# Performance work log

Measured on AMD Instinct MI355X. Metric: run time of the kernel, lower is better.

Reference implementation:

```python
import jax, jax.numpy as jnp
import numpy as np

MID = 256

def setup_inputs() -> dict:
    key = jax.random.key(0)
    ks = jax.random.split(key, 6)
    s = 1.0 / np.sqrt(MID)
    u = lambda k, shape: jax.random.uniform(k, shape, jnp.float32, -s, s)
    return {
        "W_ih": u(ks[0], (4 * MID, 2)),
        "W_hh": u(ks[1], (4 * MID, MID)),
        "b_ih": u(ks[2], (4 * MID,)),
        "b_hh": u(ks[3], (4 * MID,)),
        "W_out": u(ks[4], (1, MID)),
        "b_out": u(ks[5], (1,)),
        "sequence_dim": 48,
        "sequence_num": 512,
    }

def reference(W_ih, W_hh, b_ih, b_hh, W_out, b_out, sequence_dim, sequence_num):
    # obs is 2-D -> torch nn.LSTM treats it as UNBATCHED: (L=sequence_num, H_in=2),
    # hidden state (mid,) per layer, carried across outer iterations.
    N = sequence_num
    mid = W_hh.shape[1]
    b = b_ih + b_hh  # fuse the two LSTM biases

    def lstm(hc, obs):
        # obs: (N, 2) time-major unbatched sequence
        def step(carry, x):
            h, c = carry
            g = W_ih @ x + W_hh @ h + b          # (4*mid,)
            i, f, gg, o = jnp.split(g, 4)         # torch gate order i,f,g,o
            c = jax.nn.sigmoid(f) * c + jax.nn.sigmoid(i) * jnp.tanh(gg)
            h = jax.nn.sigmoid(o) * jnp.tanh(c)
            return (h, c), h
        hc, hs = jax.lax.scan(step, hc, obs)
        return hc, hs                              # hs: (N, mid)

    def outer(carry, k):
        hc, samp, prob = carry
        obs = jnp.concatenate([samp, prob], axis=1)  # (N, 2)
        hc, hs = lstm(hc, obs)
        p = jax.nn.sigmoid(hs @ W_out.T + b_out)     # (N, 1)
        smp = jax.random.bernoulli(k, p).astype(p.dtype)
        lp = smp * jnp.log(p) + (1.0 - smp) * jnp.log1p(-p)        # Bernoulli log_prob
        ent = -(p * jnp.log(p) + (1.0 - p) * jnp.log1p(-p))        # Bernoulli entropy
        return (hc, smp, p), (smp[:, 0], lp[:, 0], ent[:, 0])

    key = jax.random.key(42)
    keys = jax.random.split(key, sequence_dim - 1)
    h0 = (jnp.zeros((mid,), W_hh.dtype), jnp.zeros((mid,), W_hh.dtype))
    z = jnp.zeros((N, 1), W_hh.dtype)
    _, (ss, lps, ents) = jax.lax.scan(outer, (h0, z, z), keys)

    samples = jnp.concatenate([jnp.zeros((1, N), ss.dtype), ss], axis=0)  # (T, N)
    samples = samples.T.astype(jnp.int32)                                  # (N, T)
    logprobs = lps.sum(0)
    logprobs = logprobs - logprobs.mean()
    entropies = ents.mean(0)
    return samples, logprobs, entropies
```

## Files before the change

### kernel.cpp

```cpp
#include <hip/hip_runtime.h>
#include <stdint.h>


#define MID      256
#define NOUT     48
#define NSEQ     512
#define NOUTER   47
#define NSTEP    (NOUTER * NSEQ)
#define NBLK     16
#define MAGIC_V  0x1234ABCDu
#define LOG2E    1.4426950408889634f

__device__ __forceinline__ uint32_t rotl32(uint32_t x, int d) {
  return (x << d) | (x >> (32 - d));
}

__device__ __forceinline__ void threefry2x32(uint32_t k0, uint32_t k1,
                                             uint32_t x0, uint32_t x1,
                                             uint32_t& o0, uint32_t& o1) {
  uint32_t ks2 = k0 ^ k1 ^ 0x1BD11BDAu;
  uint32_t v0 = x0 + k0, v1 = x1 + k1;
#define TF_R(r) { v0 += v1; v1 = rotl32(v1, r); v1 ^= v0; }
  TF_R(13) TF_R(15) TF_R(26) TF_R(6)
  v0 += k1;  v1 += ks2 + 1u;
  TF_R(17) TF_R(29) TF_R(16) TF_R(24)
  v0 += ks2; v1 += k0 + 2u;
  TF_R(13) TF_R(15) TF_R(26) TF_R(6)
  v0 += k0;  v1 += k1 + 3u;
  TF_R(17) TF_R(29) TF_R(16) TF_R(24)
  v0 += k1;  v1 += ks2 + 4u;
  TF_R(13) TF_R(15) TF_R(26) TF_R(6)
  v0 += ks2; v1 += k0 + 5u;
#undef TF_R
  o0 = v0; o1 = v1;
}

__device__ __forceinline__ float sigf(float x) { return 1.0f / (1.0f + expf(-x)); }

__device__ __forceinline__ uint64_t packht(float h, uint32_t tag) {
  return ((uint64_t)tag << 32) | (uint64_t)__float_as_uint(h);
}

__global__ __launch_bounds__(256, 1)
void arlstm_kernel(const float* __restrict__ W_ih, const float* __restrict__ W_hh,
                   const float* __restrict__ b_ih, const float* __restrict__ b_hh,
                   const float* __restrict__ W_out, const float* __restrict__ b_out,
                   float* __restrict__ out, uint64_t* __restrict__ ws) {
  uint64_t* h_hist = ws;
  float*    obsbuf = (float*)(ws + 512 * 256);
  uint32_t* p_prog = (uint32_t*)(obsbuf + 2 * 512 * 2);
  uint32_t* magic  = p_prog + 16;

  const int tid = threadIdx.x;
  const int blk = blockIdx.x;

  __shared__ __align__(16) float hstage[256];
  __shared__ float plds[4][64];
  __shared__ float obs_lds[2];
  __shared__ float lp_acc[512];
  __shared__ float ent_acc[512];
  __shared__ float red[256];

  if (blk == NBLK) {
    __hip_atomic_store(&h_hist[tid], 0ull, __ATOMIC_RELAXED, __HIP_MEMORY_SCOPE_AGENT);
    if (tid < 16)
      __hip_atomic_store(&p_prog[tid], 0u, __ATOMIC_RELAXED, __HIP_MEMORY_SCOPE_AGENT);
    out[(tid)       * NOUT] = 0.0f;
    out[(tid + 256) * NOUT] = 0.0f;
    lp_acc[tid] = 0.0f;  lp_acc[tid + 256] = 0.0f;
    ent_acc[tid] = 0.0f; ent_acc[tid + 256] = 0.0f;
    __threadfence();
    __syncthreads();
    if (tid == 0)
      __hip_atomic_store(magic, MAGIC_V, __ATOMIC_RELEASE, __HIP_MEMORY_SCOPE_AGENT);

    const int w    = tid >> 6;
    const int lane = tid & 63;
    const float wo0 = W_out[lane * 4 + 0], wo1 = W_out[lane * 4 + 1];
    const float wo2 = W_out[lane * 4 + 2], wo3 = W_out[lane * 4 + 3];
    const float bo = b_out[0];

    for (int s = w + 1; s <= NSTEP; s += 4) {
      const int k = (s - 1) >> 9;
      const int t = (s - 1) & 511;
      uint64_t* src = h_hist + (uint64_t)(s & 511) * 256 + lane * 4;
      uint64_t v0, v1, v2, v3;
      for (;;) {
        v0 = __hip_atomic_load(src + 0, __ATOMIC_RELAXED, __HIP_MEMORY_SCOPE_AGENT);
        v1 = __hip_atomic_load(src + 1, __ATOMIC_RELAXED, __HIP_MEMORY_SCOPE_AGENT);
        v2 = __hip_atomic_load(src + 2, __ATOMIC_RELAXED, __HIP_MEMORY_SCOPE_AGENT);
        v3 = __hip_atomic_load(src + 3, __ATOMIC_RELAXED, __HIP_MEMORY_SCOPE_AGENT);
        int ok = ((uint32_t)(v0 >> 32) == (uint32_t)s) &
                 ((uint32_t)(v1 >> 32) == (uint32_t)s) &
                 ((uint32_t)(v2 >> 32) == (uint32_t)s) &
                 ((uint32_t)(v3 >> 32) == (uint32_t)s);
        if (__all(ok)) break;
      }
      float zp = fmaf(__uint_as_float((uint32_t)v0), wo0,
                 fmaf(__uint_as_float((uint32_t)v1), wo1,
                 fmaf(__uint_as_float((uint32_t)v2), wo2,
                      __uint_as_float((uint32_t)v3) * wo3)));
      zp += __shfl_xor(zp, 1);
      zp += __shfl_xor(zp, 2);
      zp += __shfl_xor(zp, 4);
      zp += __shfl_xor(zp, 8);
      zp += __shfl_xor(zp, 16);
      zp += __shfl_xor(zp, 32);
      const float p = sigf(zp + bo);

      uint32_t ka, kb, c1, c2;
      threefry2x32(0u, 42u, 0u, (uint32_t)k, ka, kb);
      threefry2x32(ka, kb, 0u, (uint32_t)t, c1, c2);
      const uint32_t bits = c1 ^ c2;
      const float u = __uint_as_float((bits >> 9) | 0x3f800000u) - 1.0f;
      const float smp = (u < p) ? 1.0f : 0.0f;

      if (lane == 0) {
        uint32_t* ob = (uint32_t*)(obsbuf + ((k + 1) & 1) * (512 * 2) + t * 2);
        __hip_atomic_store(&ob[0], __float_as_uint(smp), __ATOMIC_RELAXED, __HIP_MEMORY_SCOPE_AGENT);
        __hip_atomic_store(&ob[1], __float_as_uint(p),   __ATOMIC_RELAXED, __HIP_MEMORY_SCOPE_AGENT);
        __hip_atomic_store(&p_prog[w], (uint32_t)s, __ATOMIC_RELEASE, __HIP_MEMORY_SCOPE_AGENT);
        out[t * NOUT + (k + 1)] = smp;
        const float lg = logf(p), lg1 = log1pf(-p);
        lp_acc[t]  += (smp > 0.5f) ? lg : lg1;
        ent_acc[t] -= (p * lg + (1.0f - p) * lg1);
      }
    }
    __syncthreads();
    red[tid] = lp_acc[tid] + lp_acc[tid + 256];
    __syncthreads();
    for (int off = 128; off > 0; off >>= 1) {
      if (tid < off) red[tid] += red[tid + off];
      __syncthreads();
    }
    const float mean = red[0] * (1.0f / 512.0f);
    out[24576 + tid]        = lp_acc[tid]        - mean;
    out[24576 + 256 + tid]  = lp_acc[tid + 256]  - mean;
    out[25088 + tid]        = ent_acc[tid]       * (1.0f / 47.0f);
    out[25088 + 256 + tid]  = ent_acc[tid + 256] * (1.0f / 47.0f);
  } else {
    const int part = tid >> 6;
    const int r    = tid & 63;
    const int gate = r >> 4;
    const int jloc = r & 15;
    const int row  = gate * 256 + blk * 16 + jloc;

    float wreg[64];
#pragma unroll
    for (int c = 0; c < 64; ++c)
      wreg[c] = W_hh[row * 256 + part * 64 + c];

    float bb = 0.f, wx0 = 0.f, wx1 = 0.f, mconst = 0.f, ml = 0.f, ad = 0.f;
    if (tid < 64) {
      const int g4 = tid >> 4;
      const int rr = g4 * 256 + blk * 16 + (tid & 15);
      bb  = b_ih[rr] + b_hh[rr];
      wx0 = W_ih[rr * 2 + 0];
      wx1 = W_ih[rr * 2 + 1];
      mconst = (g4 == 2) ? (-2.0f * LOG2E) : (-LOG2E);
      ml     = (g4 == 2) ? 2.0f : 1.0f;
      ad     = (g4 == 2) ? -1.0f : 0.0f;
    }

    if (tid == 0) {
      while (__hip_atomic_load(magic, __ATOMIC_ACQUIRE, __HIP_MEMORY_SCOPE_AGENT) != MAGIC_V) {}
    }
    __syncthreads();

    float c_st = 0.0f;
    const int jglob = blk * 16 + (tid & 15);

    for (int s = 1; s <= NSTEP; ++s) {
      const int k = (s - 1) >> 9;
      const int t = (s - 1) & 511;

      float samp = 0.0f, pv = 0.0f;
      if (tid == 255 && k > 0) {
        const uint32_t X = (uint32_t)((k - 1) * 512 + t + 1);
        while (__hip_atomic_load(&p_prog[t & 3], __ATOMIC_ACQUIRE, __HIP_MEMORY_SCOPE_AGENT) < X) {}
        uint32_t* ob = (uint32_t*)(obsbuf + (k & 1) * (512 * 2) + t * 2);
        samp = __uint_as_float(__hip_atomic_load(&ob[0], __ATOMIC_RELAXED, __HIP_MEMORY_SCOPE_AGENT));
        pv   = __uint_as_float(__hip_atomic_load(&ob[1], __ATOMIC_RELAXED, __HIP_MEMORY_SCOPE_AGENT));
      }

      {
        uint64_t* src = h_hist + (uint64_t)((s - 1) & 511) * 256 + tid;
        const uint32_t want = (uint32_t)(s - 1);
        uint64_t v = __hip_atomic_load(src, __ATOMIC_RELAXED, __HIP_MEMORY_SCOPE_AGENT);
        if ((uint32_t)(v >> 32) != want) {
          uint64_t a = __hip_atomic_load(src, __ATOMIC_RELAXED, __HIP_MEMORY_SCOPE_AGENT);
          uint64_t b = __hip_atomic_load(src, __ATOMIC_RELAXED, __HIP_MEMORY_SCOPE_AGENT);
          for (;;) {
            if ((uint32_t)(a >> 32) == want) { v = a; break; }
            a = __hip_atomic_load(src, __ATOMIC_RELAXED, __HIP_MEMORY_SCOPE_AGENT);
            if ((uint32_t)(b >> 32) == want) { v = b; break; }
            b = __hip_atomic_load(src, __ATOMIC_RELAXED, __HIP_MEMORY_SCOPE_AGENT);
          }
        }
        hstage[tid] = __uint_as_float((uint32_t)v);
      }
      if (tid == 255) { obs_lds[0] = samp; obs_lds[1] = pv; }
      __syncthreads();

      float a0 = 0.f, a1 = 0.f, a2 = 0.f, a3 = 0.f;
      const float4* hs4 = (const float4*)(hstage + part * 64);
#pragma unroll
      for (int i = 0; i < 16; ++i) {
        const float4 hv = hs4[i];
        a0 = fmaf(wreg[4 * i + 0], hv.x, a0);
        a1 = fmaf(wreg[4 * i + 1], hv.y, a1);
        a2 = fmaf(wreg[4 * i + 2], hv.z, a2);
        a3 = fmaf(wreg[4 * i + 3], hv.w, a3);
      }
      plds[part][r] = (a0 + a1) + (a2 + a3);
      __syncthreads();

      if (tid < 64) {
        const float sx = obs_lds[0], px = obs_lds[1];
        const float base = wx0 * sx + wx1 * px + bb;
        const float gv = ((plds[0][tid] + plds[1][tid]) +
                          (plds[2][tid] + plds[3][tid])) + base;
        const float e   = __builtin_amdgcn_exp2f(gv * mconst);
        const float y   = __builtin_amdgcn_rcpf(1.0f + e);
        const float act = __builtin_fmaf(ml, y, ad);
        const int j = tid & 15;
        const float a_f = __shfl(act, j + 16, 64);
        const float a_g = __shfl(act, j + 32, 64);
        const float a_o = __shfl(act, j + 48, 64);
        if (tid < 16) {
          const float t1 = a_f * c_st;
          const float t2 = act * a_g;
          c_st = t1 + t2;
          const float ec = __builtin_amdgcn_exp2f(c_st * (-2.0f * LOG2E));
          const float yc = __builtin_amdgcn_rcpf(1.0f + ec);
          const float th = __builtin_fmaf(2.0f, yc, -1.0f);
          const float hnew = a_o * th;
          __hip_atomic_store(&h_hist[(uint64_t)(s & 511) * 256 + jglob],
                             packht(hnew, (uint32_t)s),
                             __ATOMIC_RELAXED, __HIP_MEMORY_SCOPE_AGENT);
        }
      }
    }
  }
}

extern "C" void kernel_launch(void* const* d_in, const int* in_sizes, int n_in,
                              void* d_out, int out_size, void* d_ws, size_t ws_size,
                              hipStream_t stream) {
  const float* W_ih  = (const float*)d_in[0];
  const float* W_hh  = (const float*)d_in[1];
  const float* b_ih  = (const float*)d_in[2];
  const float* b_hh  = (const float*)d_in[3];
  const float* W_out = (const float*)d_in[4];
  const float* b_out = (const float*)d_in[5];
  float* out = (float*)d_out;
  uint64_t* ws = (uint64_t*)d_ws;

  arlstm_kernel<<<dim3(NBLK + 1), dim3(256), 0, stream>>>(
      W_ih, W_hh, b_ih, b_hh, W_out, b_out, out, ws);
}
```

Before: 31.82 ms.

## Remove second block barrier via in-wave gate reduction and prefetched observation ring

Each wave now owns four hidden units across all four gates, so the K-split partial sums are combined with wave shuffles instead of an LDS exchange and a second __syncthreads per step. Observations from the sampler block are prefetched 16 steps ahead by one wave into a double-buffered LDS ring, which takes the p_prog spin-wait off the critical path. The h stage is double-buffered, and a block writes its own new h values straight into LDS rather than re-reading them from global memory. In exchange the indexing and prefetch-phase logic are more intricate, which raises the risk of ordering bugs.

```diff
diff --git a/kernel.cpp b/kernel.cpp
--- a/kernel.cpp
+++ b/kernel.cpp
@@ -10,6 +10,8 @@
 #define NBLK     16
 #define MAGIC_V  0x1234ABCDu
 #define LOG2E    1.4426950408889634f
+
+#define LD_REL(p) __hip_atomic_load((p), __ATOMIC_RELAXED, __HIP_MEMORY_SCOPE_AGENT)
 
 __device__ __forceinline__ uint32_t rotl32(uint32_t x, int d) {
   return (x << d) | (x >> (32 - d));
@@ -50,13 +52,13 @@
   float*    obsbuf = (float*)(ws + 512 * 256);
   uint32_t* p_prog = (uint32_t*)(obsbuf + 2 * 512 * 2);
   uint32_t* magic  = p_prog + 16;
+  uint64_t* ob64   = (uint64_t*)obsbuf;
 
   const int tid = threadIdx.x;
   const int blk = blockIdx.x;
 
-  __shared__ __align__(16) float hstage[256];
-  __shared__ float plds[4][64];
-  __shared__ float obs_lds[2];
+  __shared__ __align__(16) float hstage[2][256];
+  __shared__ __align__(16) float ring[2][16][2];
   __shared__ float lp_acc[512];
   __shared__ float ent_acc[512];
   __shared__ float red[256];
@@ -86,10 +88,10 @@
       uint64_t* src = h_hist + (uint64_t)(s & 511) * 256 + lane * 4;
       uint64_t v0, v1, v2, v3;
       for (;;) {
-        v0 = __hip_atomic_load(src + 0, __ATOMIC_RELAXED, __HIP_MEMORY_SCOPE_AGENT);
-        v1 = __hip_atomic_load(src + 1, __ATOMIC_RELAXED, __HIP_MEMORY_SCOPE_AGENT);
-        v2 = __hip_atomic_load(src + 2, __ATOMIC_RELAXED, __HIP_MEMORY_SCOPE_AGENT);
-        v3 = __hip_atomic_load(src + 3, __ATOMIC_RELAXED, __HIP_MEMORY_SCOPE_AGENT);
+        v0 = LD_REL(src + 0);
+        v1 = LD_REL(src + 1);
+        v2 = LD_REL(src + 2);
+        v3 = LD_REL(src + 3);
         int ok = ((uint32_t)(v0 >> 32) == (uint32_t)s) &
                  ((uint32_t)(v1 >> 32) == (uint32_t)s) &
                  ((uint32_t)(v2 >> 32) == (uint32_t)s) &
@@ -139,27 +141,30 @@
     out[25088 + tid]        = ent_acc[tid]       * (1.0f / 47.0f);
     out[25088 + 256 + tid]  = ent_acc[tid + 256] * (1.0f / 47.0f);
   } else {
-    const int part = tid >> 6;
-    const int r    = tid & 63;
-    const int gate = r >> 4;
-    const int jloc = r & 15;
-    const int row  = gate * 256 + blk * 16 + jloc;
+    const int lane6 = tid & 63;
+    const int wv    = tid >> 6;
+    const int p     = lane6 & 3;
+    const int js    = (lane6 >> 2) & 3;
+    const int gate  = lane6 >> 4;
+    const int jl    = 4 * wv + js;
+    const int jglob = blk * 16 + jl;
+    const int rr    = gate * 256 + blk * 16 + jl;
 
     float wreg[64];
 #pragma unroll
     for (int c = 0; c < 64; ++c)
-      wreg[c] = W_hh[row * 256 + part * 64 + c];
-
-    float bb = 0.f, wx0 = 0.f, wx1 = 0.f, mconst = 0.f, ml = 0.f, ad = 0.f;
-    if (tid < 64) {
-      const int g4 = tid >> 4;
-      const int rr = g4 * 256 + blk * 16 + (tid & 15);
-      bb  = b_ih[rr] + b_hh[rr];
-      wx0 = W_ih[rr * 2 + 0];
-      wx1 = W_ih[rr * 2 + 1];
-      mconst = (g4 == 2) ? (-2.0f * LOG2E) : (-LOG2E);
-      ml     = (g4 == 2) ? 2.0f : 1.0f;
-      ad     = (g4 == 2) ? -1.0f : 0.0f;
+      wreg[c] = W_hh[rr * 256 + p * 64 + c];
+
+    const float bb  = b_ih[rr] + b_hh[rr];
+    const float wx0 = W_ih[rr * 2 + 0];
+    const float wx1 = W_ih[rr * 2 + 1];
+    const float mconst = (gate == 2) ? (-2.0f * LOG2E) : (-LOG2E);
+    const float ml     = (gate == 2) ? 2.0f : 1.0f;
+    const float ad     = (gate == 2) ? -1.0f : 0.0f;
+
+    if (tid < 16) {
+      ring[0][tid][0] = 0.f; ring[0][tid][1] = 0.f;
+      ring[1][tid][0] = 0.f; ring[1][tid][1] = 0.f;
     }
 
     if (tid == 0) {
@@ -168,42 +173,68 @@
     __syncthreads();
 
     float c_st = 0.0f;
-    const int jglob = blk * 16 + (tid & 15);
+    const bool own = (tid >= blk * 16) && (tid < blk * 16 + 16);
+
+    int      pf_tgt = 0, pf_need = 0;
+    uint32_t pf_ppv = 0;
+    uint64_t pf_ov  = 0;
 
     for (int s = 1; s <= NSTEP; ++s) {
-      const int k = (s - 1) >> 9;
-      const int t = (s - 1) & 511;
-
-      float samp = 0.0f, pv = 0.0f;
-      if (tid == 255 && k > 0) {
-        const uint32_t X = (uint32_t)((k - 1) * 512 + t + 1);
-        while (__hip_atomic_load(&p_prog[t & 3], __ATOMIC_ACQUIRE, __HIP_MEMORY_SCOPE_AGENT) < X) {}
-        uint32_t* ob = (uint32_t*)(obsbuf + (k & 1) * (512 * 2) + t * 2);
-        samp = __uint_as_float(__hip_atomic_load(&ob[0], __ATOMIC_RELAXED, __HIP_MEMORY_SCOPE_AGENT));
-        pv   = __uint_as_float(__hip_atomic_load(&ob[1], __ATOMIC_RELAXED, __HIP_MEMORY_SCOPE_AGENT));
-      }
-
-      {
+      const int ph = (s - 1) & 15;
+
+      if (wv == 3) {
+        if (ph == 0) {
+          pf_tgt  = s + 16 + lane6;
+          pf_need = 0;
+          if (lane6 < 16 && pf_tgt > NSEQ && pf_tgt <= NSTEP) {
+            pf_need = pf_tgt - NSEQ;
+            pf_ppv  = LD_REL(&p_prog[(pf_need - 1) & 3]);
+          }
+        } else if (ph == 1) {
+          bool ok = (pf_need == 0) || (pf_ppv >= (uint32_t)pf_need);
+          while (!__all(ok)) {
+            if (!ok) pf_ppv = LD_REL(&p_prog[(pf_need - 1) & 3]);
+            ok = (pf_need == 0) || (pf_ppv >= (uint32_t)pf_need);
+          }
+          pf_ov = 0;
+          if (lane6 < 16 && pf_need != 0) {
+            const int kk = (pf_tgt - 1) >> 9;
+            const int tt = (pf_tgt - 1) & 511;
+            pf_ov = LD_REL(ob64 + (kk & 1) * 512 + tt);
+          }
+        } else if (ph == 2) {
+          if (lane6 < 16) {
+            const int par = (((s - 3) >> 4) + 1) & 1;
+            ring[par][lane6][0] = __uint_as_float((uint32_t)pf_ov);
+            ring[par][lane6][1] = __uint_as_float((uint32_t)(pf_ov >> 32));
+          }
+        }
+      }
+
+      if (s == 1 || !own) {
         uint64_t* src = h_hist + (uint64_t)((s - 1) & 511) * 256 + tid;
         const uint32_t want = (uint32_t)(s - 1);
-        uint64_t v = __hip_atomic_load(src, __ATOMIC_RELAXED, __HIP_MEMORY_SCOPE_AGENT);
+        uint64_t v = LD_REL(src);
         if ((uint32_t)(v >> 32) != want) {
-          uint64_t a = __hip_atomic_load(src, __ATOMIC_RELAXED, __HIP_MEMORY_SCOPE_AGENT);
-          uint64_t b = __hip_atomic_load(src, __ATOMIC_RELAXED, __HIP_MEMORY_SCOPE_AGENT);
+          uint64_t q0 = LD_REL(src), q1 = LD_REL(src);
+          uint64_t q2 = LD_REL(src), q3 = LD_REL(src);
           for (;;) {
-            if ((uint32_t)(a >> 32) == want) { v = a; break; }
-            a = __hip_atomic_load(src, __ATOMIC_RELAXED, __HIP_MEMORY_SCOPE_AGENT);
-            if ((uint32_t)(b >> 32) == want) { v = b; break; }
-            b = __hip_atomic_load(src, __ATOMIC_RELAXED, __HIP_MEMORY_SCOPE_AGENT);
+            if ((uint32_t)(q0 >> 32) == want) { v = q0; break; }
+            q0 = LD_REL(src);
+            if ((uint32_t)(q1 >> 32) == want) { v = q1; break; }
+            q1 = LD_REL(src);
+            if ((uint32_t)(q2 >> 32) == want) { v = q2; break; }
+            q2 = LD_REL(src);
+            if ((uint32_t)(q3 >> 32) == want) { v = q3; break; }
+            q3 = LD_REL(src);
           }
         }
-        hstage[tid] = __uint_as_float((uint32_t)v);
-      }
-      if (tid == 255) { obs_lds[0] = samp; obs_lds[1] = pv; }
+        hstage[s & 1][tid] = __uint_as_float((uint32_t)v);
+      }
       __syncthreads();
 
       float a0 = 0.f, a1 = 0.f, a2 = 0.f, a3 = 0.f;
-      const float4* hs4 = (const float4*)(hstage + part * 64);
+      const float4* hs4 = (const float4*)&hstage[s & 1][p * 64];
 #pragma unroll
       for (int i = 0; i < 16; ++i) {
         const float4 hv = hs4[i];
@@ -212,29 +243,32 @@
         a2 = fmaf(wreg[4 * i + 2], hv.z, a2);
         a3 = fmaf(wreg[4 * i + 3], hv.w, a3);
       }
-      plds[part][r] = (a0 + a1) + (a2 + a3);
-      __syncthreads();
-
-      if (tid < 64) {
-        const float sx = obs_lds[0], px = obs_lds[1];
-        const float base = wx0 * sx + wx1 * px + bb;
-        const float gv = ((plds[0][tid] + plds[1][tid]) +
-                          (plds[2][tid] + plds[3][tid])) + base;
-        const float e   = __builtin_amdgcn_exp2f(gv * mconst);
-        const float y   = __builtin_amdgcn_rcpf(1.0f + e);
-        const float act = __builtin_fmaf(ml, y, ad);
-        const int j = tid & 15;
-        const float a_f = __shfl(act, j + 16, 64);
-        const float a_g = __shfl(act, j + 32, 64);
-        const float a_o = __shfl(act, j + 48, 64);
-        if (tid < 16) {
-          const float t1 = a_f * c_st;
-          const float t2 = act * a_g;
-          c_st = t1 + t2;
-          const float ec = __builtin_amdgcn_exp2f(c_st * (-2.0f * LOG2E));
-          const float yc = __builtin_amdgcn_rcpf(1.0f + ec);
-          const float th = __builtin_fmaf(2.0f, yc, -1.0f);
-          const float hnew = a_o * th;
+      float gp = (a0 + a1) + (a2 + a3);
+      gp += __shfl_xor(gp, 1);
+      gp += __shfl_xor(gp, 2);
+
+      const float sx = ring[((s - 1) >> 4) & 1][ph][0];
+      const float px = ring[((s - 1) >> 4) & 1][ph][1];
+      const float gv = gp + (wx0 * sx + wx1 * px + bb);
+
+      const float e   = __builtin_amdgcn_exp2f(gv * mconst);
+      const float y   = __builtin_amdgcn_rcpf(1.0f + e);
+      const float act = __builtin_fmaf(ml, y, ad);
+
+      const float a_f = __shfl(act, (lane6 & 15) + 16, 64);
+      const float a_g = __shfl(act, (lane6 & 15) + 32, 64);
+      const float a_o = __shfl(act, (lane6 & 15) + 48, 64);
+
+      if (lane6 < 16) {
+        const float t1 = a_f * c_st;
+        const float t2 = act * a_g;
+        c_st = t1 + t2;
+        const float ec = __builtin_amdgcn_exp2f(c_st * (-2.0f * LOG2E));
+        const float yc = __builtin_amdgcn_rcpf(1.0f + ec);
+        const float th = __builtin_fmaf(2.0f, yc, -1.0f);
+        const float hnew = a_o * th;
+        if (p == 0) {
+          hstage[(s + 1) & 1][jglob] = hnew;
           __hip_atomic_store(&h_hist[(uint64_t)(s & 511) * 256 + jglob],
                              packht(hnew, (uint32_t)s),
                              __ATOMIC_RELAXED, __HIP_MEMORY_SCOPE_AGENT);
```

New measurement: 39.33 ms. 1.24x slower.
